# Optimization experiments

Measured on AMD Instinct MI355X. Metric: run time of the kernel, lower is better.

## Reference

```python
import jax, jax.numpy as jnp
import numpy as np

HEAD_DIM = 128
N_HEADS = 32
N_KV = 8
EPS = 1e-6


def setup_inputs() -> dict:
    key = jax.random.key(0)
    ks = jax.random.split(key, 8)
    B, S, H = 1, 2048, 2560
    hidden_states = jax.random.normal(ks[0], (B, S, H), dtype=jnp.float32)
    # rotary embeddings (any values work for a math reference)
    pos = jnp.arange(S, dtype=jnp.float32)[:, None]
    inv_freq = 1.0 / (10000.0 ** (jnp.arange(0, HEAD_DIM, 2, dtype=jnp.float32) / HEAD_DIM))
    ang = pos * inv_freq[None, :]            # [S, HEAD_DIM/2]
    emb = jnp.concatenate([ang, ang], axis=-1)  # [S, HEAD_DIM]
    cos = jnp.cos(emb)[None]                 # [1, S, HEAD_DIM]
    sin = jnp.sin(emb)[None]
    sc = 0.02
    Wq = jax.random.normal(ks[1], (N_HEADS * HEAD_DIM, H), dtype=jnp.float32) * sc
    Wk = jax.random.normal(ks[2], (N_KV * HEAD_DIM, H), dtype=jnp.float32) * sc
    Wv = jax.random.normal(ks[3], (N_KV * HEAD_DIM, H), dtype=jnp.float32) * sc
    Wo = jax.random.normal(ks[4], (H, N_HEADS * HEAD_DIM), dtype=jnp.float32) * sc
    q_norm_w = jnp.ones((HEAD_DIM,), dtype=jnp.float32)
    k_norm_w = jnp.ones((HEAD_DIM,), dtype=jnp.float32)
    return dict(hidden_states=hidden_states, cos=cos, sin=sin,
                Wq=Wq, Wk=Wk, Wv=Wv, Wo=Wo,
                q_norm_w=q_norm_w, k_norm_w=k_norm_w)


def _rms_norm(x, w):
    var = jnp.mean(x * x, axis=-1, keepdims=True)
    return x * jax.lax.rsqrt(var + EPS) * w


def _rotate_half(x):
    x1, x2 = jnp.split(x, 2, axis=-1)
    return jnp.concatenate([-x2, x1], axis=-1)


def reference(hidden_states, cos, sin, Wq, Wk, Wv, Wo, q_norm_w, k_norm_w):
    B, S, H = hidden_states.shape
    scale = HEAD_DIM ** -0.5
    # projections -> [B, heads, S, D]
    q = (hidden_states @ Wq.T).reshape(B, S, N_HEADS, HEAD_DIM)
    k = (hidden_states @ Wk.T).reshape(B, S, N_KV, HEAD_DIM)
    v = (hidden_states @ Wv.T).reshape(B, S, N_KV, HEAD_DIM)
    q = _rms_norm(q, q_norm_w).transpose(0, 2, 1, 3)   # [B, 32, S, D]
    k = _rms_norm(k, k_norm_w).transpose(0, 2, 1, 3)   # [B, 8, S, D]
    v = v.transpose(0, 2, 1, 3)
    # RoPE (cos/sin broadcast over heads via [:, None])
    c = cos[:, None]
    s = sin[:, None]
    q = q * c + _rotate_half(q) * s
    k = k * c + _rotate_half(k) * s
    # GQA: expand kv heads (repeat_kv)
    rep = N_HEADS // N_KV
    k = jnp.repeat(k, rep, axis=1)  # [B, 32, S, D]
    v = jnp.repeat(v, rep, axis=1)
    # causal SDPA (prefill => is_causal=True, full-length cache)
    scores = jnp.einsum('bhqd,bhkd->bhqk', q, k) * scale
    causal = jnp.tril(jnp.ones((S, S), dtype=bool))
    scores = jnp.where(causal, scores, jnp.finfo(scores.dtype).min)
    probs = jax.nn.softmax(scores, axis=-1)
    out = jnp.einsum('bhqk,bhkd->bhqd', probs, v)      # [B, 32, S, D]
    out = out.transpose(0, 2, 1, 3).reshape(B, S, N_HEADS * HEAD_DIM)
    return out @ Wo.T
```

## Files before the change

kernel.cpp:

```cpp
#include <hip/hip_runtime.h>
#include <hip/hip_bf16.h>

#define S_LEN   2048
#define HID     2560
#define NH      32
#define NKV     8
#define HD      128
#define QDIM    (NH*HD)
#define KVDIM   (NKV*HD)

typedef __attribute__((ext_vector_type(8))) short short8;
typedef __attribute__((ext_vector_type(4))) float f32x4;

__device__ __forceinline__ unsigned short f2bf(float f) {
    unsigned u = __float_as_uint(f);
    u += 0x7fffu + ((u >> 16) & 1u);
    return (unsigned short)(u >> 16);
}
__device__ __forceinline__ float bf2f(unsigned short s) {
    return __uint_as_float(((unsigned)s) << 16);
}
__device__ __forceinline__ unsigned pk2bf(float a, float b) {
    __hip_bfloat162 h = __float22bfloat162_rn(make_float2(a, b));
    union { __hip_bfloat162 h; unsigned u; } c; c.h = h; return c.u;
}
__device__ __forceinline__ void gload16(const void* g, void* l) {
    __builtin_amdgcn_global_load_lds(
        (const __attribute__((address_space(1))) unsigned int*)g,
        (__attribute__((address_space(3))) unsigned int*)l, 16, 0, 0);
}

#define N4_HS  (S_LEN*HID/4)
#define N4_WQ  (QDIM*HID/4)
#define N4_WKV (KVDIM*HID/4)
__global__ __launch_bounds__(256) void cvt4(
    const float* __restrict__ hs, const float* __restrict__ Wq,
    const float* __restrict__ Wk, const float* __restrict__ Wv,
    unsigned short* __restrict__ hsB, unsigned short* __restrict__ WqB,
    unsigned short* __restrict__ WkB, unsigned short* __restrict__ WvB)
{
    int i = blockIdx.x * 256 + threadIdx.x;
    const float* s; unsigned short* d;
    if (i < N4_HS)                          { s = hs; d = hsB; }
    else if (i < N4_HS + N4_WQ)             { i -= N4_HS; s = Wq; d = WqB; }
    else if (i < N4_HS + N4_WQ + N4_WKV)    { i -= N4_HS + N4_WQ; s = Wk; d = WkB; }
    else                                    { i -= N4_HS + N4_WQ + N4_WKV; s = Wv; d = WvB; }
    float4 v = ((const float4*)s)[i];
    uint2 o;
    o.x = pk2bf(v.x, v.y); o.y = pk2bf(v.z, v.w);
    ((uint2*)d)[i] = o;
}

__global__ __launch_bounds__(256) void cvt_f32_bf16(
    const float* __restrict__ s, unsigned short* __restrict__ d, int n4)
{
    int i = blockIdx.x * 256 + threadIdx.x;
    if (i >= n4) return;
    float4 v = ((const float4*)s)[i];
    uint2 o;
    o.x = pk2bf(v.x, v.y); o.y = pk2bf(v.z, v.w);
    ((uint2*)d)[i] = o;
}

struct GemmRegs {
    f32x4 acc[4][4];
};
__device__ __forceinline__ void gemm_core(
    const unsigned short* A, const unsigned short* B, int Kd,
    unsigned short* As, unsigned short* Bs, GemmRegs& R,
    int rowA0, int rowB0, int tid)
{
    const int lane = tid & 63;
    const int l15 = lane & 15, l4 = lane >> 4;
    const int w = tid >> 6;
    const int wr = (w >> 1) * 64, wc = (w & 1) * 64;
    const int sw = l15 & 7;

#pragma unroll
    for (int i = 0; i < 4; i++)
#pragma unroll
        for (int j = 0; j < 4; j++)
            R.acc[i][j] = (f32x4){0.f, 0.f, 0.f, 0.f};

    for (int k0 = 0; k0 < Kd; k0 += 64) {
        __syncthreads();
#pragma unroll
        for (int i = 0; i < 4; i++) {
            int tc = tid + i * 256;
            int r = tc >> 3, cl = tc & 7;
            int cg = cl ^ (r & 7);
            gload16(A + (size_t)(rowA0 + r) * Kd + k0 + cg * 8, &As[tc * 8]);
            gload16(B + (size_t)(rowB0 + r) * Kd + k0 + cg * 8, &Bs[tc * 8]);
        }
        __syncthreads();

#pragma unroll
        for (int ks = 0; ks < 2; ks++) {
            const int kc = (ks * 4 + l4) ^ sw;
            short8 af[4], bf[4];
#pragma unroll
            for (int i = 0; i < 4; i++)
                af[i] = *(const short8*)&As[(wr + i*16 + l15)*64 + kc*8];
#pragma unroll
            for (int j = 0; j < 4; j++)
                bf[j] = *(const short8*)&Bs[(wc + j*16 + l15)*64 + kc*8];
#pragma unroll
            for (int i = 0; i < 4; i++)
#pragma unroll
                for (int j = 0; j < 4; j++)
                    R.acc[i][j] = __builtin_amdgcn_mfma_f32_16x16x32_bf16(
                        af[i], bf[j], R.acc[i][j], 0, 0, 0);
        }
    }
}

__global__ __launch_bounds__(256) void gemm_bf16(
    const unsigned short* __restrict__ A, const unsigned short* __restrict__ B,
    float* __restrict__ Cf, unsigned short* __restrict__ Cb, int N, int Kd)
{
    __shared__ unsigned short As[128*64];
    __shared__ unsigned short Bs[128*64];
    const int tid = threadIdx.x;
    const int lane = tid & 63, w = tid >> 6;
    const int l15 = lane & 15, l4 = lane >> 4;
    const int wr = (w >> 1) * 64, wc = (w & 1) * 64;
    GemmRegs R;
    gemm_core(A, B, Kd, As, Bs, R, blockIdx.y * 128, blockIdx.x * 128, tid);

#pragma unroll
    for (int i = 0; i < 4; i++)
#pragma unroll
        for (int j = 0; j < 4; j++) {
            int row0 = blockIdx.y*128 + wr + i*16 + l4*4;
            int col  = blockIdx.x*128 + wc + j*16 + l15;
#pragma unroll
            for (int r = 0; r < 4; r++) {
                size_t off = (size_t)(row0 + r) * N + col;
                if (Cf) Cf[off] = R.acc[i][j][r];
                else    Cb[off] = f2bf(R.acc[i][j][r]);
            }
        }
}

__global__ __launch_bounds__(256) void gemm_qkv(
    const unsigned short* __restrict__ A,
    const unsigned short* __restrict__ Wq, const unsigned short* __restrict__ Wk,
    const unsigned short* __restrict__ Wv,
    unsigned short* __restrict__ Qo, unsigned short* __restrict__ Ko,
    unsigned short* __restrict__ VTo)
{
    __shared__ unsigned short As[128*64];
    __shared__ unsigned short Bs[128*64];
    const int bx = blockIdx.x;
    const unsigned short* B;
    if (bx < 32)      B = Wq + (size_t)bx*128*HID;
    else if (bx < 40) B = Wk + (size_t)(bx-32)*128*HID;
    else              B = Wv + (size_t)(bx-40)*128*HID;

    const int tid = threadIdx.x;
    const int lane = tid & 63, w = tid >> 6;
    const int l15 = lane & 15, l4 = lane >> 4;
    const int wr = (w >> 1) * 64, wc = (w & 1) * 64;
    GemmRegs R;
    gemm_core(A, B, HID, As, Bs, R, blockIdx.y * 128, 0, tid);

    if (bx < 40) {
        unsigned short* C; int ldc, cb;
        if (bx < 32) { C = Qo; ldc = QDIM;  cb = bx*128; }
        else         { C = Ko; ldc = KVDIM; cb = (bx-32)*128; }
#pragma unroll
        for (int i = 0; i < 4; i++)
#pragma unroll
            for (int j = 0; j < 4; j++) {
                int row0 = blockIdx.y*128 + wr + i*16 + l4*4;
                int col  = cb + wc + j*16 + l15;
#pragma unroll
                for (int r = 0; r < 4; r++)
                    C[(size_t)(row0 + r) * ldc + col] = f2bf(R.acc[i][j][r]);
            }
    } else {
        const int cbase = (bx - 40) * 128;
#pragma unroll
        for (int i = 0; i < 4; i++)
#pragma unroll
            for (int j = 0; j < 4; j++) {
                int col  = cbase + wc + j*16 + l15;
                int row0 = blockIdx.y*128 + wr + i*16 + l4*4;
                int kvhh = col >> 7, d = col & 127;
                unsigned short* p = VTo + (size_t)kvhh*HD*S_LEN + (size_t)d*S_LEN + row0;
                uint2 pk;
                pk.x = pk2bf(R.acc[i][j][0], R.acc[i][j][1]);
                pk.y = pk2bf(R.acc[i][j][2], R.acc[i][j][3]);
                *(uint2*)p = pk;
            }
    }
}

__global__ __launch_bounds__(256) void rmsnorm_rope_bf16(
    unsigned short* __restrict__ X, const float* __restrict__ w,
    const float* __restrict__ ct, const float* __restrict__ st, int nheads)
{
    int wid  = (blockIdx.x * blockDim.x + threadIdx.x) >> 6;
    int lane = threadIdx.x & 63;
    int s = wid / nheads;
    int h = wid - s * nheads;
    unsigned short* x = X + (size_t)s * (nheads * HD) + h * HD;

    float x1 = bf2f(x[lane]);
    float x2 = bf2f(x[lane + 64]);
    float ss = x1*x1 + x2*x2;
#pragma unroll
    for (int off = 32; off > 0; off >>= 1) ss += __shfl_xor(ss, off, 64);
    float r = rsqrtf(ss * (1.0f/128.0f) + 1e-6f);
    float n1 = x1 * r * w[lane];
    float n2 = x2 * r * w[lane + 64];
    float c1 = ct[s*HD + lane],      s1 = st[s*HD + lane];
    float c2 = ct[s*HD + lane + 64], s2 = st[s*HD + lane + 64];
    x[lane]      = f2bf(n1*c1 - n2*s1);
    x[lane + 64] = f2bf(n2*c2 + n1*s2);
}

__global__ __launch_bounds__(256, 3) void flash_mfma(
    const unsigned short* __restrict__ Q, const unsigned short* __restrict__ K,
    const unsigned short* __restrict__ VT, unsigned short* __restrict__ O)
{
    const int qt = 31 - (int)blockIdx.x;
    const int h = blockIdx.y, kvh = h >> 2;
    const int tid = threadIdx.x;
    const int w = tid >> 6, lane = tid & 63;
    const int l15 = lane & 15, l4 = lane >> 4;
    const int q0 = qt * 64;

    __shared__ unsigned short Ks[64*128];
    __shared__ unsigned short Vt[128*64];
    __shared__ unsigned short Ps[4*16*72];
    __shared__ float Lw[4][16];

    const float scale2 = 0.08838834764831845f * 1.4426950408889634f;
    const float M2 = 17.3f;
    unsigned short* Pw = &Ps[w * 16 * 72];
    const unsigned short* VTh = VT + (size_t)kvh * HD * S_LEN;

    short8 qa[4];
    {
        const unsigned short* qg = Q + (size_t)(q0 + w*16 + l15) * QDIM + h * HD;
#pragma unroll
        for (int ka = 0; ka < 4; ka++)
            qa[ka] = *(const short8*)(qg + ka*32 + l4*8);
    }

    const f32x4 zero = {0.f, 0.f, 0.f, 0.f};
    f32x4 accO[8];
#pragma unroll
    for (int j = 0; j < 8; j++) accO[j] = zero;
    float lsum = 0.f;

    for (int t = 0; t <= qt; t++) {
        const int c0 = t * 64;
        __syncthreads();
        {
#pragma unroll
            for (int i = 0; i < 4; i++) {
                int tc = tid + i * 256;
                int r = tc >> 4, cl = tc & 15;
                int cg = cl ^ (r & 7);
                gload16(K + (size_t)(c0 + r) * KVDIM + kvh * HD + cg * 8,
                        &Ks[tc * 8]);
            }
        }
        {
#pragma unroll
            for (int i = 0; i < 4; i++) {
                int tc = tid + i * 256;
                int r = tc >> 3, cl = tc & 7;
                int cg = cl ^ (r & 7);
                gload16(VTh + (size_t)r * S_LEN + c0 + cg * 8, &Vt[tc * 8]);
            }
        }
        __syncthreads();

        f32x4 sc[4];
#pragma unroll
        for (int mt = 0; mt < 4; mt++) sc[mt] = zero;
#pragma unroll
        for (int ka = 0; ka < 4; ka++) {
#pragma unroll
            for (int mt = 0; mt < 4; mt++) {
                int row = mt*16 + l15;
                int cs = (ka*4 + l4) ^ (row & 7);
                short8 kb = *(const short8*)&Ks[row*128 + cs*8];
                sc[mt] = __builtin_amdgcn_mfma_f32_16x16x32_bf16(kb, qa[ka], sc[mt], 0, 0, 0);
            }
        }

        const int qglob = q0 + w*16 + l15;
        const bool diag = (t == qt);
#pragma unroll
        for (int mt = 0; mt < 4; mt++) {
            float pv[4];
#pragma unroll
            for (int r = 0; r < 4; r++) {
                int kvg = c0 + mt*16 + l4*4 + r;
                float e = __builtin_amdgcn_exp2f(fmaf(sc[mt][r], scale2, -M2));
                pv[r] = (!diag || kvg <= qglob) ? e : 0.f;
                lsum += pv[r];
            }
            uint2 pk;
            pk.x = pk2bf(pv[0], pv[1]);
            pk.y = pk2bf(pv[2], pv[3]);
            *(uint2*)&Pw[l15*72 + mt*16 + l4*4] = pk;
        }

#pragma unroll
        for (int ks = 0; ks < 2; ks++) {
            short8 pf = *(const short8*)&Pw[l15*72 + ks*32 + l4*8];
            const int cs = (ks*4 + l4) ^ (l15 & 7);
#pragma unroll
            for (int dt = 0; dt < 8; dt++) {
                short8 vf = *(const short8*)&Vt[(dt*16 + l15)*64 + cs*8];
                accO[dt] = __builtin_amdgcn_mfma_f32_16x16x32_bf16(pf, vf, accO[dt], 0, 0, 0);
            }
        }
    }

    lsum += __shfl_xor(lsum, 16, 64);
    lsum += __shfl_xor(lsum, 32, 64);
    if (l4 == 0) Lw[w][l15] = lsum;
    f32x4 linv;
#pragma unroll
    for (int r = 0; r < 4; r++) linv[r] = 1.0f / Lw[w][l4*4 + r];

#pragma unroll
    for (int dt = 0; dt < 8; dt++)
#pragma unroll
        for (int r = 0; r < 4; r++) {
            int row_l = w*16 + l4*4 + r;
            O[(size_t)(q0 + row_l) * QDIM + h*HD + dt*16 + l15] =
                f2bf(accO[dt][r] * linv[r]);
        }
}

extern "C" void kernel_launch(void* const* d_in, const int* in_sizes, int n_in,
                              void* d_out, int out_size, void* d_ws, size_t ws_size,
                              hipStream_t stream)
{
    const float* hs   = (const float*)d_in[0];
    const float* cosb = (const float*)d_in[1];
    const float* sinb = (const float*)d_in[2];
    const float* Wq   = (const float*)d_in[3];
    const float* Wk   = (const float*)d_in[4];
    const float* Wv   = (const float*)d_in[5];
    const float* Wo   = (const float*)d_in[6];
    const float* qw   = (const float*)d_in[7];
    const float* kw   = (const float*)d_in[8];
    float* out = (float*)d_out;

    char* ws = (char*)d_ws;
    unsigned short* hsB = (unsigned short*)(ws);
    unsigned short* WqB = (unsigned short*)(ws + 10485760);
    unsigned short* WkB = (unsigned short*)(ws + 31457280);
    unsigned short* WvB = (unsigned short*)(ws + 36700160);
    unsigned short* KB  = (unsigned short*)(ws + 41943040);
    unsigned short* VT  = (unsigned short*)(ws + 46137344);
    unsigned short* WoB = (unsigned short*)(ws + 41943040);
    unsigned short* QB  = (unsigned short*)(ws + 62914560);
    unsigned short* CB  = (unsigned short*)(ws + 18874368);

    {
        int n4 = N4_HS + N4_WQ + 2 * N4_WKV;
        cvt4<<<(n4+255)/256, 256, 0, stream>>>(hs, Wq, Wk, Wv, hsB, WqB, WkB, WvB);
    }

    gemm_qkv<<<dim3(48, S_LEN/128), 256, 0, stream>>>(hsB, WqB, WkB, WvB, QB, KB, VT);

    rmsnorm_rope_bf16<<<S_LEN*NH/4,  256, 0, stream>>>(QB, qw, cosb, sinb, NH);
    rmsnorm_rope_bf16<<<S_LEN*NKV/4, 256, 0, stream>>>(KB, kw, cosb, sinb, NKV);

    flash_mfma<<<dim3(32, NH), 256, 0, stream>>>(QB, KB, VT, CB);

    cvt_f32_bf16<<<(HID*QDIM/4+255)/256, 256, 0, stream>>>(Wo, WoB, HID*QDIM/4);

    gemm_bf16<<<dim3(HID/128, S_LEN/128), 256, 0, stream>>>(CB, WoB, out, nullptr, HID, QDIM);
}
```

Before: 427.2 us.

## Pair causal query tiles per flash block and use 64-row output GEMM tiles

```diff
diff --git a/kernel.cpp b/kernel.cpp
--- a/kernel.cpp
+++ b/kernel.cpp
@@ -114,34 +114,6 @@
     }
 }
 
-__global__ __launch_bounds__(256) void gemm_bf16(
-    const unsigned short* __restrict__ A, const unsigned short* __restrict__ B,
-    float* __restrict__ Cf, unsigned short* __restrict__ Cb, int N, int Kd)
-{
-    __shared__ unsigned short As[128*64];
-    __shared__ unsigned short Bs[128*64];
-    const int tid = threadIdx.x;
-    const int lane = tid & 63, w = tid >> 6;
-    const int l15 = lane & 15, l4 = lane >> 4;
-    const int wr = (w >> 1) * 64, wc = (w & 1) * 64;
-    GemmRegs R;
-    gemm_core(A, B, Kd, As, Bs, R, blockIdx.y * 128, blockIdx.x * 128, tid);
-
-#pragma unroll
-    for (int i = 0; i < 4; i++)
-#pragma unroll
-        for (int j = 0; j < 4; j++) {
-            int row0 = blockIdx.y*128 + wr + i*16 + l4*4;
-            int col  = blockIdx.x*128 + wc + j*16 + l15;
-#pragma unroll
-            for (int r = 0; r < 4; r++) {
-                size_t off = (size_t)(row0 + r) * N + col;
-                if (Cf) Cf[off] = R.acc[i][j][r];
-                else    Cb[off] = f2bf(R.acc[i][j][r]);
-            }
-        }
-}
-
 __global__ __launch_bounds__(256) void gemm_qkv(
     const unsigned short* __restrict__ A,
     const unsigned short* __restrict__ Wq, const unsigned short* __restrict__ Wk,
@@ -196,6 +168,74 @@
     }
 }
 
+__global__ __launch_bounds__(256) void gemm_out(
+    const unsigned short* __restrict__ A, const unsigned short* __restrict__ B,
+    float* __restrict__ C, int N, int Kd)
+{
+    __shared__ unsigned short As[64*64];
+    __shared__ unsigned short Bs[128*64];
+    const int tid = threadIdx.x;
+    const int lane = tid & 63, w = tid >> 6;
+    const int l15 = lane & 15, l4 = lane >> 4;
+    const int wr = (w >> 1) * 32, wc = (w & 1) * 64;
+    const int rowA0 = blockIdx.y * 64, rowB0 = blockIdx.x * 128;
+    const int sw = l15 & 7;
+
+    f32x4 acc[2][4];
+#pragma unroll
+    for (int i = 0; i < 2; i++)
+#pragma unroll
+        for (int j = 0; j < 4; j++) acc[i][j] = (f32x4){0.f, 0.f, 0.f, 0.f};
+
+    for (int k0 = 0; k0 < Kd; k0 += 64) {
+        __syncthreads();
+#pragma unroll
+        for (int i = 0; i < 2; i++) {
+            int tc = tid + i * 256;
+            int r = tc >> 3, cl = tc & 7;
+            int cg = cl ^ (r & 7);
+            gload16(A + (size_t)(rowA0 + r) * Kd + k0 + cg * 8, &As[tc * 8]);
+        }
+#pragma unroll
+        for (int i = 0; i < 4; i++) {
+            int tc = tid + i * 256;
+            int r = tc >> 3, cl = tc & 7;
+            int cg = cl ^ (r & 7);
+            gload16(B + (size_t)(rowB0 + r) * Kd + k0 + cg * 8, &Bs[tc * 8]);
+        }
+        __syncthreads();
+
+#pragma unroll
+        for (int ks = 0; ks < 2; ks++) {
+            const int kc = (ks * 4 + l4) ^ sw;
+            short8 af[2], bf[4];
+#pragma unroll
+            for (int i = 0; i < 2; i++)
+                af[i] = *(const short8*)&As[(wr + i*16 + l15)*64 + kc*8];
+#pragma unroll
+            for (int j = 0; j < 4; j++)
+                bf[j] = *(const short8*)&Bs[(wc + j*16 + l15)*64 + kc*8];
+#pragma unroll
+            for (int i = 0; i < 2; i++)
+#pragma unroll
+                for (int j = 0; j < 4; j++)
+                    acc[i][j] = __builtin_amdgcn_mfma_f32_16x16x32_bf16(
+                        af[i], bf[j], acc[i][j], 0, 0, 0);
+        }
+    }
+
+#pragma unroll
+    for (int i = 0; i < 2; i++)
+#pragma unroll
+        for (int j = 0; j < 4; j++) {
+            int row0 = rowA0 + wr + i*16 + l4*4;
+            int col  = rowB0 + wc + j*16 + l15;
+#pragma unroll
+            for (int r = 0; r < 4; r++)
+                C[(size_t)(row0 + r) * N + col] = acc[i][j][r];
+        }
+}
+
 __global__ __launch_bounds__(256) void rmsnorm_rope_bf16(
     unsigned short* __restrict__ X, const float* __restrict__ w,
     const float* __restrict__ ct, const float* __restrict__ st, int nheads)
@@ -224,12 +264,11 @@
     const unsigned short* __restrict__ Q, const unsigned short* __restrict__ K,
     const unsigned short* __restrict__ VT, unsigned short* __restrict__ O)
 {
-    const int qt = 31 - (int)blockIdx.x;
+    const int pb = blockIdx.x;
     const int h = blockIdx.y, kvh = h >> 2;
     const int tid = threadIdx.x;
     const int w = tid >> 6, lane = tid & 63;
     const int l15 = lane & 15, l4 = lane >> 4;
-    const int q0 = qt * 64;
 
     __shared__ unsigned short Ks[64*128];
     __shared__ unsigned short Vt[128*64];
@@ -241,103 +280,109 @@
     unsigned short* Pw = &Ps[w * 16 * 72];
     const unsigned short* VTh = VT + (size_t)kvh * HD * S_LEN;
 
-    short8 qa[4];
-    {
-        const unsigned short* qg = Q + (size_t)(q0 + w*16 + l15) * QDIM + h * HD;
-#pragma unroll
-        for (int ka = 0; ka < 4; ka++)
-            qa[ka] = *(const short8*)(qg + ka*32 + l4*8);
+#pragma unroll 1
+    for (int phase = 0; phase < 2; phase++) {
+        const int qt = phase ? pb : (31 - pb);
+        const int q0 = qt * 64;
+
+        short8 qa[4];
+        {
+            const unsigned short* qg = Q + (size_t)(q0 + w*16 + l15) * QDIM + h * HD;
+#pragma unroll
+            for (int ka = 0; ka < 4; ka++)
+                qa[ka] = *(const short8*)(qg + ka*32 + l4*8);
+        }
+
+        const f32x4 zero = {0.f, 0.f, 0.f, 0.f};
+        f32x4 accO[8];
+#pragma unroll
+        for (int j = 0; j < 8; j++) accO[j] = zero;
+        float lsum = 0.f;
+
+        for (int t = 0; t <= qt; t++) {
+            const int c0 = t * 64;
+            __syncthreads();
+            {
+#pragma unroll
+                for (int i = 0; i < 4; i++) {
+                    int tc = tid + i * 256;
+                    int r = tc >> 4, cl = tc & 15;
+                    int cg = cl ^ (r & 7);
+                    gload16(K + (size_t)(c0 + r) * KVDIM + kvh * HD + cg * 8,
+                            &Ks[tc * 8]);
+                }
+            }
+            {
+#pragma unroll
+                for (int i = 0; i < 4; i++) {
+                    int tc = tid + i * 256;
+                    int r = tc >> 3, cl = tc & 7;
+                    int cg = cl ^ (r & 7);
+                    gload16(VTh + (size_t)r * S_LEN + c0 + cg * 8, &Vt[tc * 8]);
+                }
+            }
+            __syncthreads();
+
+            f32x4 sc[4];
+#pragma unroll
+            for (int mt = 0; mt < 4; mt++) sc[mt] = zero;
+#pragma unroll
+            for (int ka = 0; ka < 4; ka++) {
+#pragma unroll
+                for (int mt = 0; mt < 4; mt++) {
+                    int row = mt*16 + l15;
+                    int cs = (ka*4 + l4) ^ (row & 7);
+                    short8 kb = *(const short8*)&Ks[row*128 + cs*8];
+                    sc[mt] = __builtin_amdgcn_mfma_f32_16x16x32_bf16(kb, qa[ka], sc[mt], 0, 0, 0);
+                }
+            }
+
+            const int qglob = q0 + w*16 + l15;
+            const bool diag = (t == qt);
+#pragma unroll
+            for (int mt = 0; mt < 4; mt++) {
+                float pv[4];
+#pragma unroll
+                for (int r = 0; r < 4; r++) {
+                    int kvg = c0 + mt*16 + l4*4 + r;
+                    float e = __builtin_amdgcn_exp2f(fmaf(sc[mt][r], scale2, -M2));
+                    pv[r] = (!diag || kvg <= qglob) ? e : 0.f;
+                    lsum += pv[r];
+                }
+                uint2 pk;
+                pk.x = pk2bf(pv[0], pv[1]);
+                pk.y = pk2bf(pv[2], pv[3]);
+                *(uint2*)&Pw[l15*72 + mt*16 + l4*4] = pk;
+            }
+
+#pragma unroll
+            for (int ks = 0; ks < 2; ks++) {
+                short8 pf = *(const short8*)&Pw[l15*72 + ks*32 + l4*8];
+                const int cs = (ks*4 + l4) ^ (l15 & 7);
+#pragma unroll
+                for (int dt = 0; dt < 8; dt++) {
+                    short8 vf = *(const short8*)&Vt[(dt*16 + l15)*64 + cs*8];
+                    accO[dt] = __builtin_amdgcn_mfma_f32_16x16x32_bf16(pf, vf, accO[dt], 0, 0, 0);
+                }
+            }
+        }
+
+        lsum += __shfl_xor(lsum, 16, 64);
+        lsum += __shfl_xor(lsum, 32, 64);
+        if (l4 == 0) Lw[w][l15] = lsum;
+        f32x4 linv;
+#pragma unroll
+        for (int r = 0; r < 4; r++) linv[r] = 1.0f / Lw[w][l4*4 + r];
+
+#pragma unroll
+        for (int dt = 0; dt < 8; dt++)
+#pragma unroll
+            for (int r = 0; r < 4; r++) {
+                int row_l = w*16 + l4*4 + r;
+                O[(size_t)(q0 + row_l) * QDIM + h*HD + dt*16 + l15] =
+                    f2bf(accO[dt][r] * linv[r]);
+            }
     }
-
-    const f32x4 zero = {0.f, 0.f, 0.f, 0.f};
-    f32x4 accO[8];
-#pragma unroll
-    for (int j = 0; j < 8; j++) accO[j] = zero;
-    float lsum = 0.f;
-
-    for (int t = 0; t <= qt; t++) {
-        const int c0 = t * 64;
-        __syncthreads();
-        {
-#pragma unroll
-            for (int i = 0; i < 4; i++) {
-                int tc = tid + i * 256;
-                int r = tc >> 4, cl = tc & 15;
-                int cg = cl ^ (r & 7);
-                gload16(K + (size_t)(c0 + r) * KVDIM + kvh * HD + cg * 8,
-                        &Ks[tc * 8]);
-            }
-        }
-        {
-#pragma unroll
-            for (int i = 0; i < 4; i++) {
-                int tc = tid + i * 256;
-                int r = tc >> 3, cl = tc & 7;
-                int cg = cl ^ (r & 7);
-                gload16(VTh + (size_t)r * S_LEN + c0 + cg * 8, &Vt[tc * 8]);
-            }
-        }
-        __syncthreads();
-
-        f32x4 sc[4];
-#pragma unroll
-        for (int mt = 0; mt < 4; mt++) sc[mt] = zero;
-#pragma unroll
-        for (int ka = 0; ka < 4; ka++) {
-#pragma unroll
-            for (int mt = 0; mt < 4; mt++) {
-                int row = mt*16 + l15;
-                int cs = (ka*4 + l4) ^ (row & 7);
-                short8 kb = *(const short8*)&Ks[row*128 + cs*8];
-                sc[mt] = __builtin_amdgcn_mfma_f32_16x16x32_bf16(kb, qa[ka], sc[mt], 0, 0, 0);
-            }
-        }
-
-        const int qglob = q0 + w*16 + l15;
-        const bool diag = (t == qt);
-#pragma unroll
-        for (int mt = 0; mt < 4; mt++) {
-            float pv[4];
-#pragma unroll
-            for (int r = 0; r < 4; r++) {
-                int kvg = c0 + mt*16 + l4*4 + r;
-                float e = __builtin_amdgcn_exp2f(fmaf(sc[mt][r], scale2, -M2));
-                pv[r] = (!diag || kvg <= qglob) ? e : 0.f;
-                lsum += pv[r];
-            }
-            uint2 pk;
-            pk.x = pk2bf(pv[0], pv[1]);
-            pk.y = pk2bf(pv[2], pv[3]);
-            *(uint2*)&Pw[l15*72 + mt*16 + l4*4] = pk;
-        }
-
-#pragma unroll
-        for (int ks = 0; ks < 2; ks++) {
-            short8 pf = *(const short8*)&Pw[l15*72 + ks*32 + l4*8];
-            const int cs = (ks*4 + l4) ^ (l15 & 7);
-#pragma unroll
-            for (int dt = 0; dt < 8; dt++) {
-                short8 vf = *(const short8*)&Vt[(dt*16 + l15)*64 + cs*8];
-                accO[dt] = __builtin_amdgcn_mfma_f32_16x16x32_bf16(pf, vf, accO[dt], 0, 0, 0);
-            }
-        }
-    }
-
-    lsum += __shfl_xor(lsum, 16, 64);
-    lsum += __shfl_xor(lsum, 32, 64);
-    if (l4 == 0) Lw[w][l15] = lsum;
-    f32x4 linv;
-#pragma unroll
-    for (int r = 0; r < 4; r++) linv[r] = 1.0f / Lw[w][l4*4 + r];
-
-#pragma unroll
-    for (int dt = 0; dt < 8; dt++)
-#pragma unroll
-        for (int r = 0; r < 4; r++) {
-            int row_l = w*16 + l4*4 + r;
-            O[(size_t)(q0 + row_l) * QDIM + h*HD + dt*16 + l15] =
-                f2bf(accO[dt][r] * linv[r]);
-        }
 }
 
 extern "C" void kernel_launch(void* const* d_in, const int* in_sizes, int n_in,
@@ -376,9 +421,9 @@
     rmsnorm_rope_bf16<<<S_LEN*NH/4,  256, 0, stream>>>(QB, qw, cosb, sinb, NH);
     rmsnorm_rope_bf16<<<S_LEN*NKV/4, 256, 0, stream>>>(KB, kw, cosb, sinb, NKV);
 
-    flash_mfma<<<dim3(32, NH), 256, 0, stream>>>(QB, KB, VT, CB);
+    flash_mfma<<<dim3(16, NH), 256, 0, stream>>>(QB, KB, VT, CB);
 
     cvt_f32_bf16<<<(HID*QDIM/4+255)/256, 256, 0, stream>>>(Wo, WoB, HID*QDIM/4);
 
-    gemm_bf16<<<dim3(HID/128, S_LEN/128), 256, 0, stream>>>(CB, WoB, out, nullptr, HID, QDIM);
-}
+    gemm_out<<<dim3(HID/128, S_LEN/64), 256, 0, stream>>>(CB, WoB, out, HID, QDIM);
+}
```

Measured after the change: 385.8 us. 9.7% less time.
